# Performance work log

Measured on AMD Instinct MI355X. Metric: run time of the kernel, lower is better.

The kernel has to match this reference:

```python
import jax, jax.numpy as jnp
import numpy as np

N, C, H, W = 8, 19, 512, 512
BORDER_DILATE = 5
BORDER_POWER = 0.5
BORDER_WEIGHT = 1.0
IGNORE = 255


def setup_inputs() -> dict:
    key = jax.random.key(0)
    k1, k2 = jax.random.split(key)
    slices = jax.random.normal(k1, (N, C, H, W), dtype=jnp.float32)
    targets = jax.random.randint(k2, (N, 1, H, W), 0, C).astype(jnp.int64)
    return {"slices": slices, "targets": targets}


def class_boundaries(m):
    # m: bool (N, K, H, W); XOR of vertical/horizontal neighbors, padded like torch
    tb = m[:, :, 1:, :] ^ m[:, :, :-1, :]          # pad bottom row with 0
    lr = m[:, :, :, 1:] ^ m[:, :, :, :-1]          # pad leftmost column with 0
    tb = jnp.pad(tb, ((0, 0), (0, 0), (0, 1), (0, 0)))
    lr = jnp.pad(lr, ((0, 0), (0, 0), (0, 0), (1, 0)))
    return tb | lr


def _min_scan_axis(d, axis):
    # forward then backward chamfer pass d[i] = min(d[i], d[i -/+ 1] + 1) along `axis`
    x = jnp.moveaxis(d, axis, 0)

    def step(carry, row):
        new = jnp.minimum(row, carry + 1.0)
        return new, new

    _, fwd = jax.lax.scan(step, x[0], x[1:])
    x = jnp.concatenate([x[:1], fwd], axis=0)
    _, bwd = jax.lax.scan(step, x[-1], x[:-1][::-1])
    x = jnp.concatenate([bwd[::-1], x[-1:]], axis=0)
    return jnp.moveaxis(x, 0, axis)


def distance_matrix(border):
    # border: bool (N, K, H, W). Penalty matches torch.tensor((N,1,H,W)).sum()
    penalty = jnp.float32(N + 1 + H + W)
    d = jnp.where(border, 0.0, penalty)
    d = _min_scan_axis(d, 2)   # H forward + backward
    d = _min_scan_axis(d, 3)   # W forward + backward
    return jax.nn.relu(d - jnp.float32(BORDER_DILATE))


def _forward(slices, targets):
    t = targets[:, 0]  # (N, H, W)
    # cross-entropy, reduction='sum', ignore_index
    logp = jax.nn.log_softmax(slices, axis=1)
    valid = t != IGNORE
    t_safe = jnp.where(valid, t, 0)
    picked = jnp.take_along_axis(logp, t_safe[:, None], axis=1)[:, 0]  # (N,H,W)
    ce = -jnp.sum(jnp.where(valid, picked, 0.0))

    # border loss: vectorized over all class ids (torch loops over unique targets)
    sm = jax.nn.softmax(slices, axis=1)                      # (N,C,H,W)
    pred = jnp.argmax(slices, axis=1, keepdims=True)         # (N,1,H,W)
    cls = jnp.arange(C)[None, :, None, None]
    pred_oh = pred == cls                                    # (N,C,H,W) bool
    tgt_oh = targets == cls                                  # (N,C,H,W) bool
    pred_b = class_boundaries(pred_oh).astype(sm.dtype)
    tgt_d = distance_matrix(class_boundaries(tgt_oh))
    present = jnp.any(tgt_oh, axis=(0, 2, 3)).astype(sm.dtype)  # only ids in targets
    border = jnp.sum(sm * pred_b * tgt_d * present[None, :, None, None])

    return ce + jnp.float32(BORDER_WEIGHT) * border ** jnp.float32(BORDER_POWER)


def reference(slices, targets):
    return _forward(slices, targets)
```

## Files before the change

kernel.cpp:

```cpp
#include <hip/hip_runtime.h>

#define NN 8
#define CC 19
#define HH 512
#define WW 512
#define HW (HH*WW)
#define NPIX (NN*HW)
#define NPLANE (NN*CC)
#define BIGV (1<<20)
#define M7 0x7F7F7F7Fu

__device__ unsigned char g_tT[NPIX];
__device__ unsigned char g_pred[NPIX];
__device__ float g_lse[NPIX];
__device__ unsigned char g_inter[(size_t)NPLANE*HW];
__device__ float g_ce;
__device__ float g_part[64][16];
__device__ unsigned int g_present_mask;

__device__ __forceinline__ unsigned int eqz(unsigned int x) {
  unsigned int y = (x & M7) + M7;
  return ~(y | x | M7);
}

__global__ __launch_bounds__(256) void k_pixel(const float* __restrict__ slices,
                                               const int* __restrict__ targets) {
  int tid = blockIdx.x * 256 + threadIdx.x;
  int p4 = tid * 4;
  int n = p4 >> 18;
  int r = p4 & (HW - 1);
  const float4* base = (const float4*)(slices + (size_t)n * CC * HW + r);
  int4 t4 = ((const int4*)targets)[tid];

  float4 x = base[0];
  float m0 = x.x, m1 = x.y, m2 = x.z, m3 = x.w;
  int a0 = 0, a1 = 0, a2 = 0, a3 = 0;
  float s0 = __expf(x.x), s1 = __expf(x.y), s2 = __expf(x.z), s3 = __expf(x.w);
  float p0 = (t4.x == 0) ? x.x : 0.f;
  float p1 = (t4.y == 0) ? x.y : 0.f;
  float p2 = (t4.z == 0) ? x.z : 0.f;
  float p3 = (t4.w == 0) ? x.w : 0.f;

#pragma unroll
  for (int c = 1; c < CC; ++c) {
    float4 xc = base[(size_t)c * (HW / 4)];
    if (xc.x > m0) { m0 = xc.x; a0 = c; }
    if (xc.y > m1) { m1 = xc.y; a1 = c; }
    if (xc.z > m2) { m2 = xc.z; a2 = c; }
    if (xc.w > m3) { m3 = xc.w; a3 = c; }
    s0 += __expf(xc.x);
    s1 += __expf(xc.y);
    s2 += __expf(xc.z);
    s3 += __expf(xc.w);
    p0 = (c == t4.x) ? xc.x : p0;
    p1 = (c == t4.y) ? xc.y : p1;
    p2 = (c == t4.z) ? xc.z : p2;
    p3 = (c == t4.w) ? xc.w : p3;
  }
  float l0 = __logf(s0), l1 = __logf(s1);
  float l2 = __logf(s2), l3 = __logf(s3);

  float ce_local = 0.f;
  if (t4.x != 255) ce_local += l0 - p0;
  if (t4.y != 255) ce_local += l1 - p1;
  if (t4.z != 255) ce_local += l2 - p2;
  if (t4.w != 255) ce_local += l3 - p3;

  unsigned int msk = 0u;
  if ((unsigned)t4.x < CC) msk |= 1u << t4.x;
  if ((unsigned)t4.y < CC) msk |= 1u << t4.y;
  if ((unsigned)t4.z < CC) msk |= 1u << t4.z;
  if ((unsigned)t4.w < CC) msk |= 1u << t4.w;

  ((float4*)g_lse)[tid] = make_float4(l0, l1, l2, l3);
  ((uchar4*)g_pred)[tid] = make_uchar4((unsigned char)a0, (unsigned char)a1,
                                       (unsigned char)a2, (unsigned char)a3);
  int h = (p4 >> 9) & 511;
  int w = p4 & 511;
  unsigned char* tT = g_tT + ((size_t)n << 18) + (size_t)w * HH + h;
  tT[0]        = (unsigned char)t4.x;
  tT[HH]       = (unsigned char)t4.y;
  tT[2 * HH]   = (unsigned char)t4.z;
  tT[3 * HH]   = (unsigned char)t4.w;

  __shared__ float sred[256];
  __shared__ unsigned int smsk[256];
  sred[threadIdx.x] = ce_local;
  smsk[threadIdx.x] = msk;
  __syncthreads();
  for (int s = 128; s > 0; s >>= 1) {
    if (threadIdx.x < s) {
      sred[threadIdx.x] += sred[threadIdx.x + s];
      smsk[threadIdx.x] |= smsk[threadIdx.x + s];
    }
    __syncthreads();
  }
  if (threadIdx.x == 0) {
    atomicAdd(&g_ce, sred[0]);
    atomicOr(&g_present_mask, smsk[0]);
  }
}

__global__ __launch_bounds__(512, 4) void k_hscan() {
  int plane = blockIdx.x >> 3;
  int wt = blockIdx.x & 7;
  int hc = threadIdx.x >> 6;
  int wl = threadIdx.x & 63;
  int c = plane % CC;
  int n = plane / CC;
  int w = wt * 64 + wl;
  const unsigned char* colC = g_tT + ((size_t)n << 18) + (size_t)w * HH + hc * 64;

  uint4 ca = *(const uint4*)(colC);
  uint4 cb = *(const uint4*)(colC + 16);
  uint4 cc2 = *(const uint4*)(colC + 32);
  uint4 cd = *(const uint4*)(colC + 48);
  unsigned int cw[16];
  cw[0]=ca.x; cw[1]=ca.y; cw[2]=ca.z; cw[3]=ca.w;
  cw[4]=cb.x; cw[5]=cb.y; cw[6]=cb.z; cw[7]=cb.w;
  cw[8]=cc2.x; cw[9]=cc2.y; cw[10]=cc2.z; cw[11]=cc2.w;
  cw[12]=cd.x; cw[13]=cd.y; cw[14]=cd.z; cw[15]=cd.w;

  unsigned int lw[16];
#pragma unroll
  for (int i = 0; i < 16; ++i) lw[i] = __shfl_up(cw[i], 1, 64);
  if (wl == 0) {
    if (w > 0) {
      const unsigned char* colL = colC - HH;
      uint4 la = *(const uint4*)(colL);
      uint4 lb = *(const uint4*)(colL + 16);
      uint4 lc = *(const uint4*)(colL + 32);
      uint4 ld = *(const uint4*)(colL + 48);
      lw[0]=la.x; lw[1]=la.y; lw[2]=la.z; lw[3]=la.w;
      lw[4]=lb.x; lw[5]=lb.y; lw[6]=lb.z; lw[7]=lb.w;
      lw[8]=lc.x; lw[9]=lc.y; lw[10]=lc.z; lw[11]=lc.w;
      lw[12]=ld.x; lw[13]=ld.y; lw[14]=ld.z; lw[15]=ld.w;
    } else {
#pragma unroll
      for (int i = 0; i < 16; ++i) lw[i] = cw[i];
    }
  }

  __shared__ unsigned char s_edge[8][64];
  s_edge[hc][wl] = (unsigned char)(cw[0] & 255u);
  __syncthreads();
  unsigned int tnl = (hc < 7) ? (unsigned int)s_edge[hc + 1][wl]
                              : ((cw[15] >> 24) & 255u);

  unsigned int bc = (unsigned int)c * 0x01010101u;
  int v[64];
  int prev = BIGV;
#pragma unroll
  for (int i = 0; i < 16; ++i) {
    unsigned int cwi = cw[i];
    unsigned int nxt = (i < 15) ? (cw[i + 1] & 255u) : tnl;
    unsigned int tnw = (cwi >> 8) | (nxt << 24);
    unsigned int zc = eqz(cwi ^ bc);
    unsigned int zn = eqz(tnw ^ bc);
    unsigned int zl = eqz(lw[i] ^ bc);
    unsigned int bb = (zc ^ zn) | (zc ^ zl);
#pragma unroll
    for (int k = 0; k < 4; ++k) {
      int bit = (int)((bb >> (8 * k + 7)) & 1u);
      prev = min(bit ? 0 : 255, prev + 1);
      v[4 * i + k] = prev;
    }
  }

  __shared__ int s_car[8][64];
  s_car[hc][wl] = v[63];
  __syncthreads();
  int F = BIGV;
#pragma unroll
  for (int i = 0; i < 7; ++i)
    if (i < hc) F = min(s_car[i][wl] + 1, F + 64);
#pragma unroll
  for (int k = 0; k < 64; ++k) v[k] = min(v[k], F + k);

#pragma unroll
  for (int k = 62; k >= 0; --k) v[k] = min(v[k], v[k + 1] + 1);

  __syncthreads();
  s_car[hc][wl] = v[0];
  __syncthreads();
  int B = BIGV;
#pragma unroll
  for (int j = 7; j >= 1; --j)
    if (j > hc) B = min(s_car[j][wl] + 1, B + 64);

  unsigned char* outb = g_inter + (((size_t)plane * 8 + wt) * HH + hc * 64) * 64 + wl;
#pragma unroll
  for (int k = 0; k < 64; ++k) {
    int outv = min(v[k], B + (63 - k));
    outb[(size_t)k * 64] = (unsigned char)outv;
  }
}

__global__ __launch_bounds__(512) void k_wscan(const float* __restrict__ slices) {
  int plane = blockIdx.x >> 6;
  int hg = blockIdx.x & 63;
  int wv = threadIdx.x >> 6;
  int lane = threadIdx.x & 63;
  int h = hg * 8 + wv;
  int c = plane % CC;
  int n = plane / CC;

  const unsigned char* rowp =
      g_inter + (((size_t)plane * 8 + (lane >> 3)) * HH + h) * 64 + (lane & 7) * 8;
  uint2 r8 = *(const uint2*)rowp;

  int d0[8];
#pragma unroll
  for (int k = 0; k < 4; ++k) {
    d0[k]     = (int)((r8.x >> (k * 8)) & 255u);
    d0[k + 4] = (int)((r8.y >> (k * 8)) & 255u);
  }
  int ls[8];
  ls[0] = d0[0];
#pragma unroll
  for (int k = 1; k < 8; ++k) ls[k] = min(d0[k], ls[k - 1] + 1);
  int u = ls[7] - 8 * lane;
#pragma unroll
  for (int o = 1; o < 64; o <<= 1) {
    int t = __shfl_up(u, o, 64);
    if (lane >= o) u = min(u, t);
  }
  int cf = __shfl_up(u, 1, 64);
  int carry = (lane == 0) ? BIGV : cf + 8 * (lane - 1);
  int f[8];
#pragma unroll
  for (int k = 0; k < 8; ++k) f[k] = min(ls[k], carry + k + 1);
  int bs[8];
  bs[7] = f[7];
#pragma unroll
  for (int k = 6; k >= 0; --k) bs[k] = min(f[k], bs[k + 1] + 1);
  int mm = bs[0] + 8 * lane;
#pragma unroll
  for (int o = 1; o < 64; o <<= 1) {
    int t = __shfl_down(mm, o, 64);
    if (lane + o < 64) mm = min(mm, t);
  }
  int mb = __shfl_down(mm, 1, 64);
  int carryb = (lane == 63) ? BIGV : mb - 8 * lane;

  float acc = 0.f;
#pragma unroll
  for (int k = 0; k < 8; ++k) {
    int D = min(bs[k], carryb - k);
    int d = D - 5;
    if (d > 0) {
      int w = lane * 8 + k;
      int pix = (n * HH + h) * WW + w;
      int pcv = g_pred[pix];
      int pnv = (h + 1 < HH) ? g_pred[pix + WW] : pcv;
      int plv = (w > 0) ? g_pred[pix - 1] : pcv;
      bool ec = (pcv == c);
      if ((ec != (pnv == c)) || (ec != (plv == c))) {
        float x = slices[((size_t)n * CC + c) * HW + (size_t)h * WW + w];
        float smv = __expf(x - g_lse[pix]);
        acc += smv * (float)d;
      }
    }
  }

#pragma unroll
  for (int o = 32; o > 0; o >>= 1) acc += __shfl_down(acc, o, 64);
  if (lane == 0) {
    float pres = (g_present_mask >> c) & 1u ? 1.f : 0.f;
    atomicAdd(&g_part[blockIdx.x & 63][0], acc * pres);
  }
}

__global__ void k_final(float* __restrict__ out) {
  int t = threadIdx.x;
  float b = g_part[t][0];
#pragma unroll
  for (int o = 32; o > 0; o >>= 1) b += __shfl_down(b, o, 64);
  if (t == 0) {
    out[0] = g_ce + sqrtf(b);
    g_ce = 0.f;
    g_present_mask = 0u;
  }
  g_part[t][0] = 0.f;
}

extern "C" void kernel_launch(void* const* d_in, const int* in_sizes, int n_in,
                              void* d_out, int out_size, void* d_ws, size_t ws_size,
                              hipStream_t stream) {
  const float* slices = (const float*)d_in[0];
  const int* targets = (const int*)d_in[1];
  float* out = (float*)d_out;
  (void)d_ws; (void)ws_size; (void)in_sizes; (void)n_in; (void)out_size;

  hipLaunchKernelGGL(k_pixel, dim3(2048), dim3(256), 0, stream, slices, targets);
  hipLaunchKernelGGL(k_hscan, dim3(NPLANE * 8), dim3(512), 0, stream);
  hipLaunchKernelGGL(k_wscan, dim3(NPLANE * 64), dim3(512), 0, stream, slices);
  hipLaunchKernelGGL(k_final, dim3(1), dim3(64), 0, stream, out);
}
```

Before: 134.6 us.

## Fuse four kernels into one persistent cooperative kernel with grid syncs

```diff
diff --git a/kernel.cpp b/kernel.cpp
--- a/kernel.cpp
+++ b/kernel.cpp
@@ -1,4 +1,7 @@
 #include <hip/hip_runtime.h>
+#include <hip/hip_cooperative_groups.h>
+
+namespace cg = cooperative_groups;
 
 #define NN 8
 #define CC 19
@@ -9,6 +12,8 @@
 #define NPLANE (NN*CC)
 #define BIGV (1<<20)
 #define M7 0x7F7F7F7Fu
+#define NBLK 256
+#define NTHR 512
 
 __device__ unsigned char g_tT[NPIX];
 __device__ unsigned char g_pred[NPIX];
@@ -23,265 +28,284 @@
   return ~(y | x | M7);
 }
 
-__global__ __launch_bounds__(256) void k_pixel(const float* __restrict__ slices,
-                                               const int* __restrict__ targets) {
-  int tid = blockIdx.x * 256 + threadIdx.x;
-  int p4 = tid * 4;
-  int n = p4 >> 18;
-  int r = p4 & (HW - 1);
-  const float4* base = (const float4*)(slices + (size_t)n * CC * HW + r);
-  int4 t4 = ((const int4*)targets)[tid];
-
-  float4 x = base[0];
-  float m0 = x.x, m1 = x.y, m2 = x.z, m3 = x.w;
-  int a0 = 0, a1 = 0, a2 = 0, a3 = 0;
-  float s0 = __expf(x.x), s1 = __expf(x.y), s2 = __expf(x.z), s3 = __expf(x.w);
-  float p0 = (t4.x == 0) ? x.x : 0.f;
-  float p1 = (t4.y == 0) ? x.y : 0.f;
-  float p2 = (t4.z == 0) ? x.z : 0.f;
-  float p3 = (t4.w == 0) ? x.w : 0.f;
-
-#pragma unroll
-  for (int c = 1; c < CC; ++c) {
-    float4 xc = base[(size_t)c * (HW / 4)];
-    if (xc.x > m0) { m0 = xc.x; a0 = c; }
-    if (xc.y > m1) { m1 = xc.y; a1 = c; }
-    if (xc.z > m2) { m2 = xc.z; a2 = c; }
-    if (xc.w > m3) { m3 = xc.w; a3 = c; }
-    s0 += __expf(xc.x);
-    s1 += __expf(xc.y);
-    s2 += __expf(xc.z);
-    s3 += __expf(xc.w);
-    p0 = (c == t4.x) ? xc.x : p0;
-    p1 = (c == t4.y) ? xc.y : p1;
-    p2 = (c == t4.z) ? xc.z : p2;
-    p3 = (c == t4.w) ? xc.w : p3;
+__global__ __launch_bounds__(NTHR, 2) void k_all(const float* __restrict__ slices,
+                                                 const int* __restrict__ targets,
+                                                 float* __restrict__ out) {
+  cg::grid_group grid = cg::this_grid();
+  const int tix = threadIdx.x;
+  const int bix = blockIdx.x;
+
+  __shared__ float sred[NTHR];
+  __shared__ unsigned int smsk[NTHR];
+  __shared__ unsigned char s_edge[8][64];
+  __shared__ int s_car[8][64];
+
+  {
+    float ce_local = 0.f;
+    unsigned int msk = 0u;
+    for (int u = bix * NTHR + tix; u < NPIX / 4; u += NBLK * NTHR) {
+      int p4 = u * 4;
+      int n = p4 >> 18;
+      int r = p4 & (HW - 1);
+      const float4* base = (const float4*)(slices + (size_t)n * CC * HW + r);
+      int4 t4 = ((const int4*)targets)[u];
+
+      float4 x = base[0];
+      float m0 = x.x, m1 = x.y, m2 = x.z, m3 = x.w;
+      int a0 = 0, a1 = 0, a2 = 0, a3 = 0;
+      float s0 = __expf(x.x), s1 = __expf(x.y), s2 = __expf(x.z), s3 = __expf(x.w);
+      float p0 = (t4.x == 0) ? x.x : 0.f;
+      float p1 = (t4.y == 0) ? x.y : 0.f;
+      float p2 = (t4.z == 0) ? x.z : 0.f;
+      float p3 = (t4.w == 0) ? x.w : 0.f;
+
+#pragma unroll
+      for (int c = 1; c < CC; ++c) {
+        float4 xc = base[(size_t)c * (HW / 4)];
+        if (xc.x > m0) { m0 = xc.x; a0 = c; }
+        if (xc.y > m1) { m1 = xc.y; a1 = c; }
+        if (xc.z > m2) { m2 = xc.z; a2 = c; }
+        if (xc.w > m3) { m3 = xc.w; a3 = c; }
+        s0 += __expf(xc.x);
+        s1 += __expf(xc.y);
+        s2 += __expf(xc.z);
+        s3 += __expf(xc.w);
+        p0 = (c == t4.x) ? xc.x : p0;
+        p1 = (c == t4.y) ? xc.y : p1;
+        p2 = (c == t4.z) ? xc.z : p2;
+        p3 = (c == t4.w) ? xc.w : p3;
+      }
+      float l0 = __logf(s0), l1 = __logf(s1);
+      float l2 = __logf(s2), l3 = __logf(s3);
+
+      if (t4.x != 255) ce_local += l0 - p0;
+      if (t4.y != 255) ce_local += l1 - p1;
+      if (t4.z != 255) ce_local += l2 - p2;
+      if (t4.w != 255) ce_local += l3 - p3;
+
+      if ((unsigned)t4.x < CC) msk |= 1u << t4.x;
+      if ((unsigned)t4.y < CC) msk |= 1u << t4.y;
+      if ((unsigned)t4.z < CC) msk |= 1u << t4.z;
+      if ((unsigned)t4.w < CC) msk |= 1u << t4.w;
+
+      ((float4*)g_lse)[u] = make_float4(l0, l1, l2, l3);
+      ((uchar4*)g_pred)[u] = make_uchar4((unsigned char)a0, (unsigned char)a1,
+                                         (unsigned char)a2, (unsigned char)a3);
+      int h = (p4 >> 9) & 511;
+      int w = p4 & 511;
+      unsigned char* tT = g_tT + ((size_t)n << 18) + (size_t)w * HH + h;
+      tT[0]      = (unsigned char)t4.x;
+      tT[HH]     = (unsigned char)t4.y;
+      tT[2 * HH] = (unsigned char)t4.z;
+      tT[3 * HH] = (unsigned char)t4.w;
+    }
+
+    sred[tix] = ce_local;
+    smsk[tix] = msk;
+    __syncthreads();
+    for (int s = NTHR / 2; s > 0; s >>= 1) {
+      if (tix < s) {
+        sred[tix] += sred[tix + s];
+        smsk[tix] |= smsk[tix + s];
+      }
+      __syncthreads();
+    }
+    if (tix == 0) {
+      atomicAdd(&g_ce, sred[0]);
+      atomicOr(&g_present_mask, smsk[0]);
+    }
   }
-  float l0 = __logf(s0), l1 = __logf(s1);
-  float l2 = __logf(s2), l3 = __logf(s3);
-
-  float ce_local = 0.f;
-  if (t4.x != 255) ce_local += l0 - p0;
-  if (t4.y != 255) ce_local += l1 - p1;
-  if (t4.z != 255) ce_local += l2 - p2;
-  if (t4.w != 255) ce_local += l3 - p3;
-
-  unsigned int msk = 0u;
-  if ((unsigned)t4.x < CC) msk |= 1u << t4.x;
-  if ((unsigned)t4.y < CC) msk |= 1u << t4.y;
-  if ((unsigned)t4.z < CC) msk |= 1u << t4.z;
-  if ((unsigned)t4.w < CC) msk |= 1u << t4.w;
-
-  ((float4*)g_lse)[tid] = make_float4(l0, l1, l2, l3);
-  ((uchar4*)g_pred)[tid] = make_uchar4((unsigned char)a0, (unsigned char)a1,
-                                       (unsigned char)a2, (unsigned char)a3);
-  int h = (p4 >> 9) & 511;
-  int w = p4 & 511;
-  unsigned char* tT = g_tT + ((size_t)n << 18) + (size_t)w * HH + h;
-  tT[0]        = (unsigned char)t4.x;
-  tT[HH]       = (unsigned char)t4.y;
-  tT[2 * HH]   = (unsigned char)t4.z;
-  tT[3 * HH]   = (unsigned char)t4.w;
-
-  __shared__ float sred[256];
-  __shared__ unsigned int smsk[256];
-  sred[threadIdx.x] = ce_local;
-  smsk[threadIdx.x] = msk;
-  __syncthreads();
-  for (int s = 128; s > 0; s >>= 1) {
-    if (threadIdx.x < s) {
-      sred[threadIdx.x] += sred[threadIdx.x + s];
-      smsk[threadIdx.x] |= smsk[threadIdx.x + s];
+
+  grid.sync();
+
+  for (int job = bix; job < NPLANE * 8; job += NBLK) {
+    int plane = job >> 3;
+    int wt = job & 7;
+    int hc = tix >> 6;
+    int wl = tix & 63;
+    int c = plane % CC;
+    int n = plane / CC;
+    int w = wt * 64 + wl;
+    const unsigned char* colC = g_tT + ((size_t)n << 18) + (size_t)w * HH + hc * 64;
+
+    uint4 ca = *(const uint4*)(colC);
+    uint4 cb = *(const uint4*)(colC + 16);
+    uint4 cc2 = *(const uint4*)(colC + 32);
+    uint4 cd = *(const uint4*)(colC + 48);
+    unsigned int cw[16];
+    cw[0]=ca.x; cw[1]=ca.y; cw[2]=ca.z; cw[3]=ca.w;
+    cw[4]=cb.x; cw[5]=cb.y; cw[6]=cb.z; cw[7]=cb.w;
+    cw[8]=cc2.x; cw[9]=cc2.y; cw[10]=cc2.z; cw[11]=cc2.w;
+    cw[12]=cd.x; cw[13]=cd.y; cw[14]=cd.z; cw[15]=cd.w;
+
+    unsigned int lw[16];
+#pragma unroll
+    for (int i = 0; i < 16; ++i) lw[i] = __shfl_up(cw[i], 1, 64);
+    if (wl == 0) {
+      if (w > 0) {
+        const unsigned char* colL = colC - HH;
+        uint4 la = *(const uint4*)(colL);
+        uint4 lb = *(const uint4*)(colL + 16);
+        uint4 lc = *(const uint4*)(colL + 32);
+        uint4 ld = *(const uint4*)(colL + 48);
+        lw[0]=la.x; lw[1]=la.y; lw[2]=la.z; lw[3]=la.w;
+        lw[4]=lb.x; lw[5]=lb.y; lw[6]=lb.z; lw[7]=lb.w;
+        lw[8]=lc.x; lw[9]=lc.y; lw[10]=lc.z; lw[11]=lc.w;
+        lw[12]=ld.x; lw[13]=ld.y; lw[14]=ld.z; lw[15]=ld.w;
+      } else {
+#pragma unroll
+        for (int i = 0; i < 16; ++i) lw[i] = cw[i];
+      }
+    }
+
+    s_edge[hc][wl] = (unsigned char)(cw[0] & 255u);
+    __syncthreads();
+    unsigned int tnl = (hc < 7) ? (unsigned int)s_edge[hc + 1][wl]
+                                : ((cw[15] >> 24) & 255u);
+
+    unsigned int bc = (unsigned int)c * 0x01010101u;
+    int v[64];
+    int prev = BIGV;
+#pragma unroll
+    for (int i = 0; i < 16; ++i) {
+      unsigned int cwi = cw[i];
+      unsigned int nxt = (i < 15) ? (cw[i + 1] & 255u) : tnl;
+      unsigned int tnw = (cwi >> 8) | (nxt << 24);
+      unsigned int zc = eqz(cwi ^ bc);
+      unsigned int zn = eqz(tnw ^ bc);
+      unsigned int zl = eqz(lw[i] ^ bc);
+      unsigned int bb = (zc ^ zn) | (zc ^ zl);
+#pragma unroll
+      for (int k = 0; k < 4; ++k) {
+        int bit = (int)((bb >> (8 * k + 7)) & 1u);
+        prev = min(bit ? 0 : 255, prev + 1);
+        v[4 * i + k] = prev;
+      }
+    }
+
+    s_car[hc][wl] = v[63];
+    __syncthreads();
+    int F = BIGV;
+#pragma unroll
+    for (int i = 0; i < 7; ++i)
+      if (i < hc) F = min(s_car[i][wl] + 1, F + 64);
+#pragma unroll
+    for (int k = 0; k < 64; ++k) v[k] = min(v[k], F + k);
+
+#pragma unroll
+    for (int k = 62; k >= 0; --k) v[k] = min(v[k], v[k + 1] + 1);
+
+    __syncthreads();
+    s_car[hc][wl] = v[0];
+    __syncthreads();
+    int B = BIGV;
+#pragma unroll
+    for (int j = 7; j >= 1; --j)
+      if (j > hc) B = min(s_car[j][wl] + 1, B + 64);
+
+    unsigned char* outb = g_inter + (((size_t)plane * 8 + wt) * HH + hc * 64) * 64 + wl;
+#pragma unroll
+    for (int k = 0; k < 64; ++k) {
+      int outv = min(v[k], B + (63 - k));
+      outb[(size_t)k * 64] = (unsigned char)outv;
     }
     __syncthreads();
   }
-  if (threadIdx.x == 0) {
-    atomicAdd(&g_ce, sred[0]);
-    atomicOr(&g_present_mask, smsk[0]);
+
+  grid.sync();
+
+  {
+    unsigned int pmask = g_present_mask;
+    int wv = tix >> 6;
+    int lane = tix & 63;
+    float acc_tot = 0.f;
+
+    for (int job = bix; job < NPLANE * 64; job += NBLK) {
+      int plane = job >> 6;
+      int hg = job & 63;
+      int h = hg * 8 + wv;
+      int c = plane % CC;
+      int n = plane / CC;
+
+      const unsigned char* rowp =
+          g_inter + (((size_t)plane * 8 + (lane >> 3)) * HH + h) * 64 + (lane & 7) * 8;
+      uint2 r8 = *(const uint2*)rowp;
+
+      int d0[8];
+#pragma unroll
+      for (int k = 0; k < 4; ++k) {
+        d0[k]     = (int)((r8.x >> (k * 8)) & 255u);
+        d0[k + 4] = (int)((r8.y >> (k * 8)) & 255u);
+      }
+      int ls[8];
+      ls[0] = d0[0];
+#pragma unroll
+      for (int k = 1; k < 8; ++k) ls[k] = min(d0[k], ls[k - 1] + 1);
+      int u = ls[7] - 8 * lane;
+#pragma unroll
+      for (int o = 1; o < 64; o <<= 1) {
+        int t = __shfl_up(u, o, 64);
+        if (lane >= o) u = min(u, t);
+      }
+      int cf = __shfl_up(u, 1, 64);
+      int carry = (lane == 0) ? BIGV : cf + 8 * (lane - 1);
+      int f[8];
+#pragma unroll
+      for (int k = 0; k < 8; ++k) f[k] = min(ls[k], carry + k + 1);
+      int bs[8];
+      bs[7] = f[7];
+#pragma unroll
+      for (int k = 6; k >= 0; --k) bs[k] = min(f[k], bs[k + 1] + 1);
+      int mm = bs[0] + 8 * lane;
+#pragma unroll
+      for (int o = 1; o < 64; o <<= 1) {
+        int t = __shfl_down(mm, o, 64);
+        if (lane + o < 64) mm = min(mm, t);
+      }
+      int mb = __shfl_down(mm, 1, 64);
+      int carryb = (lane == 63) ? BIGV : mb - 8 * lane;
+
+      float acc = 0.f;
+#pragma unroll
+      for (int k = 0; k < 8; ++k) {
+        int D = min(bs[k], carryb - k);
+        int d = D - 5;
+        if (d > 0) {
+          int w = lane * 8 + k;
+          int pix = (n * HH + h) * WW + w;
+          int pcv = g_pred[pix];
+          int pnv = (h + 1 < HH) ? g_pred[pix + WW] : pcv;
+          int plv = (w > 0) ? g_pred[pix - 1] : pcv;
+          bool ec = (pcv == c);
+          if ((ec != (pnv == c)) || (ec != (plv == c))) {
+            float x = slices[((size_t)n * CC + c) * HW + (size_t)h * WW + w];
+            float smv = __expf(x - g_lse[pix]);
+            acc += smv * (float)d;
+          }
+        }
+      }
+      float pres = ((pmask >> c) & 1u) ? 1.f : 0.f;
+      acc_tot += acc * pres;
+    }
+
+#pragma unroll
+    for (int o = 32; o > 0; o >>= 1) acc_tot += __shfl_down(acc_tot, o, 64);
+    if (lane == 0) atomicAdd(&g_part[bix & 63][0], acc_tot);
   }
-}
-
-__global__ __launch_bounds__(512, 4) void k_hscan() {
-  int plane = blockIdx.x >> 3;
-  int wt = blockIdx.x & 7;
-  int hc = threadIdx.x >> 6;
-  int wl = threadIdx.x & 63;
-  int c = plane % CC;
-  int n = plane / CC;
-  int w = wt * 64 + wl;
-  const unsigned char* colC = g_tT + ((size_t)n << 18) + (size_t)w * HH + hc * 64;
-
-  uint4 ca = *(const uint4*)(colC);
-  uint4 cb = *(const uint4*)(colC + 16);
-  uint4 cc2 = *(const uint4*)(colC + 32);
-  uint4 cd = *(const uint4*)(colC + 48);
-  unsigned int cw[16];
-  cw[0]=ca.x; cw[1]=ca.y; cw[2]=ca.z; cw[3]=ca.w;
-  cw[4]=cb.x; cw[5]=cb.y; cw[6]=cb.z; cw[7]=cb.w;
-  cw[8]=cc2.x; cw[9]=cc2.y; cw[10]=cc2.z; cw[11]=cc2.w;
-  cw[12]=cd.x; cw[13]=cd.y; cw[14]=cd.z; cw[15]=cd.w;
-
-  unsigned int lw[16];
-#pragma unroll
-  for (int i = 0; i < 16; ++i) lw[i] = __shfl_up(cw[i], 1, 64);
-  if (wl == 0) {
-    if (w > 0) {
-      const unsigned char* colL = colC - HH;
-      uint4 la = *(const uint4*)(colL);
-      uint4 lb = *(const uint4*)(colL + 16);
-      uint4 lc = *(const uint4*)(colL + 32);
-      uint4 ld = *(const uint4*)(colL + 48);
-      lw[0]=la.x; lw[1]=la.y; lw[2]=la.z; lw[3]=la.w;
-      lw[4]=lb.x; lw[5]=lb.y; lw[6]=lb.z; lw[7]=lb.w;
-      lw[8]=lc.x; lw[9]=lc.y; lw[10]=lc.z; lw[11]=lc.w;
-      lw[12]=ld.x; lw[13]=ld.y; lw[14]=ld.z; lw[15]=ld.w;
-    } else {
-#pragma unroll
-      for (int i = 0; i < 16; ++i) lw[i] = cw[i];
-    }
+
+  grid.sync();
+
+  if (bix == 0 && tix < 64) {
+    float b = g_part[tix][0];
+#pragma unroll
+    for (int o = 32; o > 0; o >>= 1) b += __shfl_down(b, o, 64);
+    if (tix == 0) {
+      out[0] = g_ce + sqrtf(b);
+      g_ce = 0.f;
+      g_present_mask = 0u;
+    }
+    g_part[tix][0] = 0.f;
   }
-
-  __shared__ unsigned char s_edge[8][64];
-  s_edge[hc][wl] = (unsigned char)(cw[0] & 255u);
-  __syncthreads();
-  unsigned int tnl = (hc < 7) ? (unsigned int)s_edge[hc + 1][wl]
-                              : ((cw[15] >> 24) & 255u);
-
-  unsigned int bc = (unsigned int)c * 0x01010101u;
-  int v[64];
-  int prev = BIGV;
-#pragma unroll
-  for (int i = 0; i < 16; ++i) {
-    unsigned int cwi = cw[i];
-    unsigned int nxt = (i < 15) ? (cw[i + 1] & 255u) : tnl;
-    unsigned int tnw = (cwi >> 8) | (nxt << 24);
-    unsigned int zc = eqz(cwi ^ bc);
-    unsigned int zn = eqz(tnw ^ bc);
-    unsigned int zl = eqz(lw[i] ^ bc);
-    unsigned int bb = (zc ^ zn) | (zc ^ zl);
-#pragma unroll
-    for (int k = 0; k < 4; ++k) {
-      int bit = (int)((bb >> (8 * k + 7)) & 1u);
-      prev = min(bit ? 0 : 255, prev + 1);
-      v[4 * i + k] = prev;
-    }
-  }
-
-  __shared__ int s_car[8][64];
-  s_car[hc][wl] = v[63];
-  __syncthreads();
-  int F = BIGV;
-#pragma unroll
-  for (int i = 0; i < 7; ++i)
-    if (i < hc) F = min(s_car[i][wl] + 1, F + 64);
-#pragma unroll
-  for (int k = 0; k < 64; ++k) v[k] = min(v[k], F + k);
-
-#pragma unroll
-  for (int k = 62; k >= 0; --k) v[k] = min(v[k], v[k + 1] + 1);
-
-  __syncthreads();
-  s_car[hc][wl] = v[0];
-  __syncthreads();
-  int B = BIGV;
-#pragma unroll
-  for (int j = 7; j >= 1; --j)
-    if (j > hc) B = min(s_car[j][wl] + 1, B + 64);
-
-  unsigned char* outb = g_inter + (((size_t)plane * 8 + wt) * HH + hc * 64) * 64 + wl;
-#pragma unroll
-  for (int k = 0; k < 64; ++k) {
-    int outv = min(v[k], B + (63 - k));
-    outb[(size_t)k * 64] = (unsigned char)outv;
-  }
-}
-
-__global__ __launch_bounds__(512) void k_wscan(const float* __restrict__ slices) {
-  int plane = blockIdx.x >> 6;
-  int hg = blockIdx.x & 63;
-  int wv = threadIdx.x >> 6;
-  int lane = threadIdx.x & 63;
-  int h = hg * 8 + wv;
-  int c = plane % CC;
-  int n = plane / CC;
-
-  const unsigned char* rowp =
-      g_inter + (((size_t)plane * 8 + (lane >> 3)) * HH + h) * 64 + (lane & 7) * 8;
-  uint2 r8 = *(const uint2*)rowp;
-
-  int d0[8];
-#pragma unroll
-  for (int k = 0; k < 4; ++k) {
-    d0[k]     = (int)((r8.x >> (k * 8)) & 255u);
-    d0[k + 4] = (int)((r8.y >> (k * 8)) & 255u);
-  }
-  int ls[8];
-  ls[0] = d0[0];
-#pragma unroll
-  for (int k = 1; k < 8; ++k) ls[k] = min(d0[k], ls[k - 1] + 1);
-  int u = ls[7] - 8 * lane;
-#pragma unroll
-  for (int o = 1; o < 64; o <<= 1) {
-    int t = __shfl_up(u, o, 64);
-    if (lane >= o) u = min(u, t);
-  }
-  int cf = __shfl_up(u, 1, 64);
-  int carry = (lane == 0) ? BIGV : cf + 8 * (lane - 1);
-  int f[8];
-#pragma unroll
-  for (int k = 0; k < 8; ++k) f[k] = min(ls[k], carry + k + 1);
-  int bs[8];
-  bs[7] = f[7];
-#pragma unroll
-  for (int k = 6; k >= 0; --k) bs[k] = min(f[k], bs[k + 1] + 1);
-  int mm = bs[0] + 8 * lane;
-#pragma unroll
-  for (int o = 1; o < 64; o <<= 1) {
-    int t = __shfl_down(mm, o, 64);
-    if (lane + o < 64) mm = min(mm, t);
-  }
-  int mb = __shfl_down(mm, 1, 64);
-  int carryb = (lane == 63) ? BIGV : mb - 8 * lane;
-
-  float acc = 0.f;
-#pragma unroll
-  for (int k = 0; k < 8; ++k) {
-    int D = min(bs[k], carryb - k);
-    int d = D - 5;
-    if (d > 0) {
-      int w = lane * 8 + k;
-      int pix = (n * HH + h) * WW + w;
-      int pcv = g_pred[pix];
-      int pnv = (h + 1 < HH) ? g_pred[pix + WW] : pcv;
-      int plv = (w > 0) ? g_pred[pix - 1] : pcv;
-      bool ec = (pcv == c);
-      if ((ec != (pnv == c)) || (ec != (plv == c))) {
-        float x = slices[((size_t)n * CC + c) * HW + (size_t)h * WW + w];
-        float smv = __expf(x - g_lse[pix]);
-        acc += smv * (float)d;
-      }
-    }
-  }
-
-#pragma unroll
-  for (int o = 32; o > 0; o >>= 1) acc += __shfl_down(acc, o, 64);
-  if (lane == 0) {
-    float pres = (g_present_mask >> c) & 1u ? 1.f : 0.f;
-    atomicAdd(&g_part[blockIdx.x & 63][0], acc * pres);
-  }
-}
-
-__global__ void k_final(float* __restrict__ out) {
-  int t = threadIdx.x;
-  float b = g_part[t][0];
-#pragma unroll
-  for (int o = 32; o > 0; o >>= 1) b += __shfl_down(b, o, 64);
-  if (t == 0) {
-    out[0] = g_ce + sqrtf(b);
-    g_ce = 0.f;
-    g_present_mask = 0u;
-  }
-  g_part[t][0] = 0.f;
 }
 
 extern "C" void kernel_launch(void* const* d_in, const int* in_sizes, int n_in,
@@ -292,8 +316,7 @@
   float* out = (float*)d_out;
   (void)d_ws; (void)ws_size; (void)in_sizes; (void)n_in; (void)out_size;
 
-  hipLaunchKernelGGL(k_pixel, dim3(2048), dim3(256), 0, stream, slices, targets);
-  hipLaunchKernelGGL(k_hscan, dim3(NPLANE * 8), dim3(512), 0, stream);
-  hipLaunchKernelGGL(k_wscan, dim3(NPLANE * 64), dim3(512), 0, stream, slices);
-  hipLaunchKernelGGL(k_final, dim3(1), dim3(64), 0, stream, out);
+  void* args[] = {(void*)&slices, (void*)&targets, (void*)&out};
+  hipLaunchCooperativeKernel((const void*)k_all, dim3(NBLK), dim3(NTHR),
+                             args, 0, stream);
 }
```

After: 332.9 us. +147.3%, slower.
